# Optimization experiments

Hardware: AMD Instinct MI355X
Metric: run time of the kernel (lower is better)

The kernel has to match this reference:

```python
import math
import jax, jax.numpy as jnp
import numpy as np

NHEAD = 4
EPS = 1e-5


def make_pe(max_len, d):
    pos = np.arange(max_len, dtype=np.float32)[:, None]
    div = np.exp(np.arange(0, d, 2, dtype=np.float32) * (-math.log(10000.0) / d))
    pe = np.zeros((max_len, d), np.float32)
    pe[:, 0::2] = np.sin(pos * div)
    pe[:, 1::2] = np.cos(pos * div)
    return jnp.asarray(pe)


def layer_norm(x, g, b):
    m = jnp.mean(x, axis=-1, keepdims=True)
    v = jnp.mean((x - m) ** 2, axis=-1, keepdims=True)
    return (x - m) / jnp.sqrt(v + EPS) * g + b


def mha(q, k, v, wq, bq, wk, bk, wv, bv, wo, bo, kmask=None):
    # q: [b, Lq, d], k/v: [b, Lk, d]
    b_, lq, d = q.shape
    lk = k.shape[1]
    hd = d // NHEAD
    qh = (q @ wq + bq).reshape(b_, lq, NHEAD, hd)
    kh = (k @ wk + bk).reshape(b_, lk, NHEAD, hd)
    vh = (v @ wv + bv).reshape(b_, lk, NHEAD, hd)
    s = jnp.einsum('bqhd,bkhd->bhqk', qh, kh) / jnp.sqrt(jnp.float32(hd))
    if kmask is not None:
        s = jnp.where(kmask[None, None, None, :], s, jnp.float32(-1e9))
    a = jax.nn.softmax(s, axis=-1)
    o = jnp.einsum('bhqk,bkhd->bqhd', a, vh).reshape(b_, lq, d)
    return o @ wo + bo


def _forward(src, in_w, in_b, dec_start,
             e_wq, e_bq, e_wk, e_bk, e_wv, e_bv, e_wo, e_bo,
             e_ln1_g, e_ln1_b, e_w1, e_b1, e_w2, e_b2, e_ln2_g, e_ln2_b,
             d_swq, d_sbq, d_swk, d_sbk, d_swv, d_sbv, d_swo, d_sbo,
             d_ln1_g, d_ln1_b,
             d_cwq, d_cbq, d_cwk, d_cbk, d_cwv, d_cbv, d_cwo, d_cbo,
             d_ln2_g, d_ln2_b,
             d_w1, d_b1, d_w2, d_b2, d_ln3_g, d_ln3_b,
             out_w, out_b, tgt_len):
    B, S = src.shape
    d = in_w.shape[1]
    T = tgt_len
    pe = make_pe(max(S, T) + 10, d)

    # ---- encoder (1 post-norm layer, relu FFN, dropout off) ----
    x = (src[..., None] @ in_w + in_b) * jnp.sqrt(jnp.float32(d))  # [B,S,d]
    x = x + pe[None, :S]
    x = layer_norm(x + mha(x, x, x, e_wq, e_bq, e_wk, e_bk, e_wv, e_bv, e_wo, e_bo), e_ln1_g, e_ln1_b)
    mem = layer_norm(x + (jax.nn.relu(x @ e_w1 + e_b1) @ e_w2 + e_b2), e_ln2_g, e_ln2_b)

    buf0 = jnp.zeros((B, T + 1, d), src.dtype).at[:, 0].set(dec_start[0, 0])
    pe_dec = pe[None, :T + 1]
    kidx = jnp.arange(T + 1)

    def step(buf, t):
        di = buf + pe_dec
        kmask = kidx <= t  # full (non-causal) attention over the t+1 valid tokens
        h = layer_norm(di + mha(di, di, di, d_swq, d_sbq, d_swk, d_sbk,
                                d_swv, d_sbv, d_swo, d_sbo, kmask=kmask),
                       d_ln1_g, d_ln1_b)
        h = layer_norm(h + mha(h, mem, mem, d_cwq, d_cbq, d_cwk, d_cbk,
                               d_cwv, d_cbv, d_cwo, d_cbo),
                       d_ln2_g, d_ln2_b)
        h = layer_norm(h + (jax.nn.relu(h @ d_w1 + d_b1) @ d_w2 + d_b2),
                       d_ln3_g, d_ln3_b)
        last = h[:, t]                       # [B,d] output at the newest position
        buf = buf.at[:, t + 1].set(last)     # feed back as next decoder token
        y = (last @ out_w + out_b)[:, 0]     # [B]
        return buf, y

    _, outs = jax.lax.scan(step, buf0, jnp.arange(T))  # outs: [T,B]
    return outs.T  # [B,T]


def setup_inputs():
    B, S, T, d, ff = 128, 512, 64, 48, 128
    ks = iter(jax.random.split(jax.random.key(0), 64))

    def w(shape, s=0.08):
        return jax.random.normal(next(ks), shape, jnp.float32) * s

    ones = lambda: jnp.ones((d,), jnp.float32)
    zeros = lambda: jnp.zeros((d,), jnp.float32)
    return dict(
        src=jax.random.normal(next(ks), (B, S), jnp.float32),
        in_w=w((1, d)), in_b=w((d,)),
        dec_start=w((1, 1, d), 1.0),
        e_wq=w((d, d)), e_bq=w((d,)), e_wk=w((d, d)), e_bk=w((d,)),
        e_wv=w((d, d)), e_bv=w((d,)), e_wo=w((d, d)), e_bo=w((d,)),
        e_ln1_g=ones(), e_ln1_b=zeros(),
        e_w1=w((d, ff)), e_b1=w((ff,)), e_w2=w((ff, d)), e_b2=w((d,)),
        e_ln2_g=ones(), e_ln2_b=zeros(),
        d_swq=w((d, d)), d_sbq=w((d,)), d_swk=w((d, d)), d_sbk=w((d,)),
        d_swv=w((d, d)), d_sbv=w((d,)), d_swo=w((d, d)), d_sbo=w((d,)),
        d_ln1_g=ones(), d_ln1_b=zeros(),
        d_cwq=w((d, d)), d_cbq=w((d,)), d_cwk=w((d, d)), d_cbk=w((d,)),
        d_cwv=w((d, d)), d_cbv=w((d,)), d_cwo=w((d, d)), d_cbo=w((d,)),
        d_ln2_g=ones(), d_ln2_b=zeros(),
        d_w1=w((d, ff)), d_b1=w((ff,)), d_w2=w((ff, d)), d_b2=w((d,)),
        d_ln3_g=ones(), d_ln3_b=zeros(),
        out_w=w((d, 1)), out_b=w((1,)),
        tgt_len=T,
    )


def reference(src, in_w, in_b, dec_start,
              e_wq, e_bq, e_wk, e_bk, e_wv, e_bv, e_wo, e_bo,
              e_ln1_g, e_ln1_b, e_w1, e_b1, e_w2, e_b2, e_ln2_g, e_ln2_b,
              d_swq, d_sbq, d_swk, d_sbk, d_swv, d_sbv, d_swo, d_sbo,
              d_ln1_g, d_ln1_b,
              d_cwq, d_cbq, d_cwk, d_cbk, d_cwv, d_cbv, d_cwo, d_cbo,
              d_ln2_g, d_ln2_b,
              d_w1, d_b1, d_w2, d_b2, d_ln3_g, d_ln3_b,
              out_w, out_b, tgt_len):
    return _forward(src, in_w, in_b, dec_start,
                    e_wq, e_bq, e_wk, e_bk, e_wv, e_bv, e_wo, e_bo,
                    e_ln1_g, e_ln1_b, e_w1, e_b1, e_w2, e_b2, e_ln2_g, e_ln2_b,
                    d_swq, d_sbq, d_swk, d_sbk, d_swv, d_sbv, d_swo, d_sbo,
                    d_ln1_g, d_ln1_b,
                    d_cwq, d_cbq, d_cwk, d_cbk, d_cwv, d_cbv, d_cwo, d_cbo,
                    d_ln2_g, d_ln2_b,
                    d_w1, d_b1, d_w2, d_b2, d_ln3_g, d_ln3_b,
                    out_w, out_b, tgt_len)
```

## Files before the change

### kernel.cpp

```cpp
#include <hip/hip_runtime.h>
#include <hip/hip_bf16.h>
#include <hip/hip_fp16.h>


constexpr int kB  = 128;
constexpr int kS  = 512;
constexpr int kT  = 64;
constexpr int kD  = 48;
constexpr int kFF = 128;
constexpr int kNH = 4;
constexpr int kHD = 12;

__device__ __forceinline__ void wsync(){
  __builtin_amdgcn_wave_barrier();
  asm volatile("" ::: "memory");
}

template<int CTRL,int RM,int BM,bool BC>
__device__ __forceinline__ float dppmov(float x, float old){
  return __builtin_bit_cast(float, __builtin_amdgcn_update_dpp(
      __builtin_bit_cast(int, old), __builtin_bit_cast(int, x), CTRL, RM, BM, BC));
}
__device__ __forceinline__ float wsum(float x){
  x += dppmov<0x111,0xf,0xf,true>(x, 0.f);
  x += dppmov<0x112,0xf,0xf,true>(x, 0.f);
  x += dppmov<0x114,0xf,0xf,true>(x, 0.f);
  x += dppmov<0x118,0xf,0xf,true>(x, 0.f);
  x += dppmov<0x142,0xa,0xf,true>(x, 0.f);
  x += dppmov<0x143,0xc,0xf,true>(x, 0.f);
  return __builtin_bit_cast(float, __builtin_amdgcn_readlane(__builtin_bit_cast(int, x), 63));
}
__device__ __forceinline__ float rowsum16(float x){
  x += dppmov<0x111,0xf,0xf,true>(x, 0.f);
  x += dppmov<0x112,0xf,0xf,true>(x, 0.f);
  x += dppmov<0x114,0xf,0xf,true>(x, 0.f);
  x += dppmov<0x118,0xf,0xf,true>(x, 0.f);
  return x;
}

__device__ __forceinline__ float pe_val(int p, int j){
  int i = j >> 1;
  float f = expf(-0.19188209108283716f * (float)(2*i));
  float a = (float)p * f;
  return (j & 1) ? cosf(a) : sinf(a);
}
__device__ __forceinline__ float pe_fast(int p, int j){
  int i = j >> 1;
  float f = __expf(-0.19188209108283716f * (float)(2*i));
  float a = (float)p * f;
  return (j & 1) ? __cosf(a) : __sinf(a);
}

typedef _Float16 h2v __attribute__((ext_vector_type(2)));
union H2U { __half2 h; h2v v; };
__device__ __forceinline__ float fdot2(__half2 a, __half2 b, float c){
#if __has_builtin(__builtin_amdgcn_fdot2)
  H2U ua, ub; ua.h=a; ub.h=b;
  return __builtin_amdgcn_fdot2(ua.v, ub.v, c, false);
#else
  float2 fa=__half22float2(a), fb=__half22float2(b);
  return fmaf(fa.y, fb.y, fmaf(fa.x, fb.x, c));
#endif
}
union F4H2 { float4 f; __half2 h[4]; };

__device__ __forceinline__ float dot48d(const __half2* x, const __half* w){
  const __half2* w2=(const __half2*)w;
  float a0=0.f,a1=0.f,a2=0.f,a3=0.f;
  #pragma unroll
  for(int c=0;c<6;c++){
    a0=fdot2(x[4*c+0],w2[4*c+0],a0);
    a1=fdot2(x[4*c+1],w2[4*c+1],a1);
    a2=fdot2(x[4*c+2],w2[4*c+2],a2);
    a3=fdot2(x[4*c+3],w2[4*c+3],a3);
  }
  return (a0+a1)+(a2+a3);
}
__device__ __forceinline__ float dot128d(const __half2* x, const __half* w){
  const __half2* w2=(const __half2*)w;
  float a0=0.f,a1=0.f,a2=0.f,a3=0.f,a4=0.f,a5=0.f,a6=0.f,a7=0.f;
  #pragma unroll
  for(int c=0;c<8;c++){
    a0=fdot2(x[8*c+0],w2[8*c+0],a0);
    a1=fdot2(x[8*c+1],w2[8*c+1],a1);
    a2=fdot2(x[8*c+2],w2[8*c+2],a2);
    a3=fdot2(x[8*c+3],w2[8*c+3],a3);
    a4=fdot2(x[8*c+4],w2[8*c+4],a4);
    a5=fdot2(x[8*c+5],w2[8*c+5],a5);
    a6=fdot2(x[8*c+6],w2[8*c+6],a6);
    a7=fdot2(x[8*c+7],w2[8*c+7],a7);
  }
  return ((a0+a1)+(a2+a3))+((a4+a5)+(a6+a7));
}

__global__ void __launch_bounds__(256) k_qkv(const float* __restrict__ src,
    const float* __restrict__ in_w, const float* __restrict__ in_b,
    float* __restrict__ X0,
    const float* __restrict__ wq, const float* __restrict__ bq,
    const float* __restrict__ wk, const float* __restrict__ bk,
    const float* __restrict__ wv, const float* __restrict__ bv,
    __half* __restrict__ Q, __half* __restrict__ K, __half* __restrict__ V,
    const float* __restrict__ swq, const float* __restrict__ swk,
    const float* __restrict__ swv, const float* __restrict__ swo,
    const float* __restrict__ cwq, const float* __restrict__ cwo,
    const float* __restrict__ dw1, const float* __restrict__ dw2,
    __half* __restrict__ Wh){
  if(blockIdx.x >= 2048){
    int idx=(blockIdx.x-2048)*256+threadIdx.x;
    if(idx>=26112) return;
    if(idx<13824){
      int m=idx/2304, e=idx%2304, j=e/48, k=e%48;
      const float* w = (m==0)?swq:((m==1)?swk:((m==2)?swv:((m==3)?swo:((m==4)?cwq:cwo))));
      Wh[m*2688 + j*56 + k] = __float2half(w[k*48+j]);
    } else if(idx<19968){
      int e=idx-13824, c=e/48, k=e%48;
      Wh[16128 + c*56 + k] = __float2half(dw1[k*128+c]);
    } else {
      int e=idx-19968, j=e/128, u=e%128;
      Wh[23296 + j*136 + u] = __float2half(dw2[u*48+j]);
    }
    return;
  }
  __shared__ __align__(16) __half W[3*2688];
  __shared__ __align__(16) float bias[3*kD];
  __shared__ __align__(16) __half2 xt2[32*24];
  int tid = threadIdx.x;
  for (int i=tid;i<3*2304;i+=256){ int m=i/2304, e=i%2304, k=e/48, j=e%48;
    const float* w = (m==0)?wq:((m==1)?wk:wv);
    W[m*2688 + j*56 + k] = __float2half(w[e]); }
  for (int i=tid;i<3*kD;i+=256){ int m=i/kD,e=i%kD;
    const float* w=(m==0)?bq:((m==1)?bk:bv); bias[i]=w[e]; }
  long row0 = (long)blockIdx.x*32;
  const float sc = 6.928203230275509f;
  for (int i=tid;i<768;i+=256){
    int r=i/24, c=i%24;
    long gr=row0+r; int s=(int)(gr&511);
    float sv=src[gr];
    float va=(sv*in_w[2*c  ]+in_b[2*c  ])*sc + pe_fast(s,2*c  );
    float vb=(sv*in_w[2*c+1]+in_b[2*c+1])*sc + pe_fast(s,2*c+1);
    ((float2*)X0)[row0*24 + i]=make_float2(va,vb);
    xt2[i]=__floats2half2_rn(va,vb);
  }
  __syncthreads();
  int r = tid>>3, c0 = tid&7;
  __half2 xr[24];
  #pragma unroll
  for(int u=0;u<24;u++) xr[u]=xt2[r*24+u];
  const float rs = 0.28867513459481287f;
  for (int c=c0; c<3*kD; c+=8){
    int m=c/kD, j=c%kD;
    float acc = bias[m*kD+j] + dot48d(xr, W + m*2688 + j*56);
    if(m==0) acc*=rs;
    __half* o = (m==0)?Q:((m==1)?K:V);
    o[(row0+r)*kD+j]=__float2half(acc);
  }
}

__global__ void __launch_bounds__(256) k_attn(const __half* __restrict__ Q,
      const __half* __restrict__ K, const __half* __restrict__ V,
      __half* __restrict__ OP, float* __restrict__ lP){
  int part = blockIdx.x & 1;
  int bh = blockIdx.x >> 1;
  int b = bh / kNH, h = bh % kNH;
  __shared__ __align__(16) __half2 Ks2[256*8];
  __shared__ __align__(16) float   Vs[256*kHD];
  int tid = threadIdx.x;
  long base = ((long)b*kS)*kD + h*kHD;
  int k0 = part<<8;
  for (int i=tid;i<256*6;i+=256){ int r=i/6, c=i%6;
    Ks2[r*8+c]=*(const __half2*)&K[base+(long)(k0+r)*kD+2*c]; }
  for (int i=tid;i<256*kHD;i+=256){ int r=i/kHD, d=i%kHD;
    Vs[i]=__half2float(V[base+(long)(k0+r)*kD+d]); }
  int q0 = tid, q1 = tid+256;
  __half2 qa2[6], qb2[6];
  {
    const __half2* qp0=(const __half2*)(Q+base+(long)q0*kD);
    const __half2* qp1=(const __half2*)(Q+base+(long)q1*kD);
    #pragma unroll
    for(int c=0;c<6;c++){ qa2[c]=qp0[c]; qb2[c]=qp1[c]; }
  }
  __syncthreads();
  float2 acc0[6], acc1[6];
  #pragma unroll
  for(int j=0;j<6;j++){ acc0[j]=make_float2(0.f,0.f); acc1[j]=make_float2(0.f,0.f); }
  float l0=0.f, l1=0.f;
  for(int k=0;k<256;k++){
    const float4* kp4=(const float4*)(Ks2+k*8);
    F4H2 u0,u1; u0.f=kp4[0]; u1.f=kp4[1];
    float sA0=0.f,sA1=0.f,sB0=0.f,sB1=0.f;
    sA0=fdot2(qa2[0],u0.h[0],sA0); sA1=fdot2(qa2[1],u0.h[1],sA1);
    sA0=fdot2(qa2[2],u0.h[2],sA0); sA1=fdot2(qa2[3],u0.h[3],sA1);
    sA0=fdot2(qa2[4],u1.h[0],sA0); sA1=fdot2(qa2[5],u1.h[1],sA1);
    sB0=fdot2(qb2[0],u0.h[0],sB0); sB1=fdot2(qb2[1],u0.h[1],sB1);
    sB0=fdot2(qb2[2],u0.h[2],sB0); sB1=fdot2(qb2[3],u0.h[3],sB1);
    sB0=fdot2(qb2[4],u1.h[0],sB0); sB1=fdot2(qb2[5],u1.h[1],sB1);
    float p0=__expf(sA0+sA1), p1=__expf(sB0+sB1);
    l0+=p0; l1+=p1;
    const float4* vp=(const float4*)(Vs+k*kHD);
    float4 v0=vp[0], v1=vp[1], v2=vp[2];
    acc0[0].x=fmaf(p0,v0.x,acc0[0].x); acc0[0].y=fmaf(p0,v0.y,acc0[0].y);
    acc0[1].x=fmaf(p0,v0.z,acc0[1].x); acc0[1].y=fmaf(p0,v0.w,acc0[1].y);
    acc0[2].x=fmaf(p0,v1.x,acc0[2].x); acc0[2].y=fmaf(p0,v1.y,acc0[2].y);
    acc0[3].x=fmaf(p0,v1.z,acc0[3].x); acc0[3].y=fmaf(p0,v1.w,acc0[3].y);
    acc0[4].x=fmaf(p0,v2.x,acc0[4].x); acc0[4].y=fmaf(p0,v2.y,acc0[4].y);
    acc0[5].x=fmaf(p0,v2.z,acc0[5].x); acc0[5].y=fmaf(p0,v2.w,acc0[5].y);
    acc1[0].x=fmaf(p1,v0.x,acc1[0].x); acc1[0].y=fmaf(p1,v0.y,acc1[0].y);
    acc1[1].x=fmaf(p1,v0.z,acc1[1].x); acc1[1].y=fmaf(p1,v0.w,acc1[1].y);
    acc1[2].x=fmaf(p1,v1.x,acc1[2].x); acc1[2].y=fmaf(p1,v1.y,acc1[2].y);
    acc1[3].x=fmaf(p1,v1.z,acc1[3].x); acc1[3].y=fmaf(p1,v1.w,acc1[3].y);
    acc1[4].x=fmaf(p1,v2.x,acc1[4].x); acc1[4].y=fmaf(p1,v2.y,acc1[4].y);
    acc1[5].x=fmaf(p1,v2.z,acc1[5].x); acc1[5].y=fmaf(p1,v2.w,acc1[5].y);
  }
  float i0=1.f/l0, i1=1.f/l1;
  const long PS=(long)kB*kNH*kS*kHD, LS=(long)kB*kNH*kS;
  long ob=((long)(b*kNH+h))*kS;
  __half2* op0=(__half2*)(OP + part*PS + (ob+q0)*kHD);
  __half2* op1=(__half2*)(OP + part*PS + (ob+q1)*kHD);
  #pragma unroll
  for(int j=0;j<6;j++){
    op0[j]=__floats2half2_rn(acc0[j].x*i0, acc0[j].y*i0);
    op1[j]=__floats2half2_rn(acc1[j].x*i1, acc1[j].y*i1);
  }
  lP[part*LS + ob + q0]=l0;
  lP[part*LS + ob + q1]=l1;
}

__global__ void __launch_bounds__(256) k_oproj_ln(const float* __restrict__ Xres,
      const __half* __restrict__ OP, const float* __restrict__ lP,
      const float* __restrict__ wo, const float* __restrict__ bo,
      const float* __restrict__ g, const float* __restrict__ bb,
      __half* __restrict__ Xout){
  __shared__ __align__(16) __half W[kD*56];
  __shared__ float bsh[kD], gs[kD], bs2[kD];
  __shared__ __align__(16) float res[32*kD];
  __shared__ __align__(16) __half2 ot2[32*24];
  __shared__ float mrow[32], rstd[32];
  int tid=threadIdx.x;
  for(int i=tid;i<kD*kD;i+=256){ int k=i/48, j=i%48; W[j*56+k]=__float2half(wo[i]); }
  if(tid<kD){ bsh[tid]=bo[tid]; gs[tid]=g[tid]; bs2[tid]=bb[tid]; }
  long row0=(long)blockIdx.x*32;
  const long PS=(long)kB*kNH*kS*kHD, LS=(long)kB*kNH*kS;
  for(int i=tid;i<768;i+=256){
    int r=i/24, c=i%24;
    long gq=row0+r; long bb2=gq>>9; long s=gq&511;
    int h=c/6; int d0=(2*c)%12;
    long li=(bb2*kNH+h)*kS+s;
    float l0=lP[li], l1=lP[li+LS];
    float inv=1.f/(l0+l1);
    long o0=li*(long)kHD+d0;
    float v0=(l0*__half2float(OP[o0  ]) + l1*__half2float(OP[o0  +PS]))*inv;
    float v1=(l0*__half2float(OP[o0+1]) + l1*__half2float(OP[o0+1+PS]))*inv;
    ot2[i]=__floats2half2_rn(v0,v1);
  }
  __syncthreads();
  int r=tid>>3, c0=tid&7;
  __half2 orow[24];
  #pragma unroll
  for(int u=0;u<24;u++) orow[u]=ot2[r*24+u];
  for(int j=c0;j<kD;j+=8){
    float acc=bsh[j]+dot48d(orow, W+j*56);
    res[r*kD+j]=Xres[row0*kD + r*kD + j]+acc;
  }
  __syncthreads();
  if(tid<32){
    float s=0.f, s2=0.f;
    for(int j=0;j<kD;j++){ float v=res[tid*kD+j]; s+=v; s2+=v*v; }
    float m=s*(1.f/kD);
    mrow[tid]=m; rstd[tid]=rsqrtf(s2*(1.f/kD)-m*m+1e-5f);
  }
  __syncthreads();
  for(int i=tid;i<32*kD;i+=256){int r2=i/kD,j=i%kD;
    Xout[row0*kD+i]=__float2half((res[i]-mrow[r2])*rstd[r2]*gs[j]+bs2[j]); }
}

__global__ void __launch_bounds__(256) k_ffn_ln(const __half* __restrict__ Xin,
   const float* __restrict__ w1, const float* __restrict__ b1,
   const float* __restrict__ w2, const float* __restrict__ b2,
   const float* __restrict__ g, const float* __restrict__ bb,
   float* __restrict__ Xout){
  __shared__ __align__(16) __half W1[kFF*56];
  __shared__ __align__(16) __half W2[kD*136];
  __shared__ float b1s[kFF], b2s[kD], gs[kD], bs2[kD];
  __shared__ __align__(16) __half xt[16*kD];
  __shared__ __align__(16) __half h1h[16*kFF];
  __shared__ __align__(16) float res[16*kD];
  __shared__ float mrow[16], rstd[16];
  int tid=threadIdx.x;
  for(int i=tid;i<kD*kFF;i+=256){ int k=i/128, c=i%128; W1[c*56+k]=__float2half(w1[i]); }
  for(int i=tid;i<kFF*kD;i+=256){ int u=i/48, j=i%48; W2[j*136+u]=__float2half(w2[i]); }
  if(tid<kFF) b1s[tid]=b1[tid];
  if(tid<kD){ b2s[tid]=b2[tid]; gs[tid]=g[tid]; bs2[tid]=bb[tid]; }
  long row0=(long)blockIdx.x*16;
  const __half2* Xp=(const __half2*)(Xin+row0*kD);
  for(int i=tid;i<384;i+=256) ((__half2*)xt)[i]=Xp[i];
  __syncthreads();
  int r=tid>>4, c0=tid&15;
  {
    __half2 xr[24];
    const __half2* xp=(const __half2*)(xt + r*kD);
    #pragma unroll
    for(int u=0;u<24;u++) xr[u]=xp[u];
    for(int c=c0;c<kFF;c+=16){
      float acc=b1s[c]+dot48d(xr, W1+c*56);
      h1h[r*kFF+c]=__float2half(fmaxf(acc,0.f));
    }
  }
  __syncthreads();
  {
    const __half2* hp=(const __half2*)(h1h + r*kFF);
    for(int j=c0;j<kD;j+=16){
      float acc=b2s[j]+dot128d(hp, W2+j*136);
      res[r*kD+j]=__half2float(xt[r*kD+j])+acc;
    }
  }
  __syncthreads();
  if(tid<16){
    float s=0.f, s2=0.f;
    for(int j=0;j<kD;j++){ float v=res[tid*kD+j]; s+=v; s2+=v*v; }
    float m=s*(1.f/kD);
    mrow[tid]=m; rstd[tid]=rsqrtf(s2*(1.f/kD)-m*m+1e-5f);
  }
  __syncthreads();
  for(int i=tid;i<16*kD;i+=256){int r2=i/kD,j=i%kD;
    Xout[row0*kD+i]=(res[i]-mrow[r2])*rstd[r2]*gs[j]+bs2[j]; }
}

__global__ void __launch_bounds__(256) k_ckv(const float* __restrict__ M,
    const float* __restrict__ wk, const float* __restrict__ bk,
    const float* __restrict__ wv, const float* __restrict__ bv,
    __half* __restrict__ Kc, __half* __restrict__ Vc){
  __shared__ __align__(16) __half W[2*2688];
  __shared__ float bias[2*kD];
  __shared__ __align__(16) __half2 xt2[32*24];
  int tid=threadIdx.x;
  for(int i=tid;i<2*2304;i+=256){ int m=i/2304, e=i%2304, k=e/48, j=e%48;
    W[m*2688 + j*56 + k] = __float2half((m?wv:wk)[e]); }
  for(int i=tid;i<2*kD;i+=256){ int m=i/kD,e=i%kD; bias[i]=(m?bv:bk)[e]; }
  long row0=(long)blockIdx.x*32;
  const float2* Mp=(const float2*)(M+row0*kD);
  for(int i=tid;i<768;i+=256){ float2 v=Mp[i]; xt2[i]=__floats2half2_rn(v.x,v.y); }
  __syncthreads();
  int r=tid>>3, c0=tid&7;
  __half2 xr[24];
  #pragma unroll
  for(int u=0;u<24;u++) xr[u]=xt2[r*24+u];
  long gr=row0+r; long bb2=gr>>9; long s=gr&511;
  for(int c=c0;c<2*kD;c+=8){
    int m=c/kD, j=c%kD;
    float acc=bias[m*kD+j]+dot48d(xr, W+m*2688+j*56);
    if(m==0) Kc[(bb2*kS+s)*kD + j]=__float2half(acc);
    else     Vc[(bb2*kD+j)*kS + s]=__float2half(acc);
  }
}

struct DecP {
  const float *dec_start, *sbq, *sbk, *sbv, *sbo, *ln1g, *ln1b,
              *cbq, *cbo, *ln2g, *ln2b, *fb1, *fb2, *ln3g, *ln3b, *ow, *ob;
};

__global__ void __launch_bounds__(256,1) k_dec(const __half* __restrict__ KT,
    const __half* __restrict__ VT, const __half* __restrict__ Wg, DecP P,
    float* __restrict__ out){
  __shared__ __align__(16) __half Wl[29824];
  __shared__ __align__(16) float peT[kT*kD];
  __shared__ __align__(16) __half KhH[kNH*kT*kHD];
  __shared__ __align__(16) float  Vh[kNH*kT*kHD];
  __shared__ __align__(16) __half qSH[kNH*kHD];
  __shared__ __align__(16) float poS[kNH][kD];
  __shared__ __align__(16) __half xvH[kD], soH[kD], h1H[kD], cqH[kD], h2H[kD];
  __shared__ __align__(16) __half f1H[kFF];
  int tid=threadIdx.x, b=blockIdx.x, wave=tid>>6, lane=tid&63;
  const float rs=0.28867513459481287f;

  for(int i=tid;i<29824/8;i+=256) ((float4*)Wl)[i]=((const float4*)Wg)[i];
  for(int i=tid;i<kT*kD;i+=256){ int tt=i/kD, j=i%kD; peT[i]=pe_val(tt,j); }

  float c_sbq=0,c_sbk=0,c_sbv=0, c_bo=0,c_cbq=0,c_cbo=0,c_fb2=0;
  float g1=0,bb1=0,g2=0,bb2=0,g3=0,bb3=0,c_ow=0, c_fb1a=0,c_fb1b=0, c_ds=0;
  if(wave==0){
    if(lane<kD){
      c_ds=P.dec_start[lane];
      c_sbq=P.sbq[lane]; c_sbk=P.sbk[lane]; c_sbv=P.sbv[lane];
      c_bo=P.sbo[lane]; c_cbq=P.cbq[lane]; c_cbo=P.cbo[lane]; c_fb2=P.fb2[lane];
      g1=P.ln1g[lane]; bb1=P.ln1b[lane];
      g2=P.ln2g[lane]; bb2=P.ln2b[lane];
      g3=P.ln3g[lane]; bb3=P.ln3b[lane];
      c_ow=P.ow[lane];
    }
    c_fb1a=P.fb1[lane]; c_fb1b=P.fb1[lane+64];
  }
  float c_ob=P.ob[0];

  __half2 Kr2[4][2][6], Vr2[4][kHD];
  {
    const __half* Kb = KT + (long)b*kS*kD;
    const __half2* Vb = (const __half2*)VT + (long)b*kD*(kS/2);
    #pragma unroll
    for(int i=0;i<4;i++){
      int sp = lane + 64*i;
      #pragma unroll
      for(int e=0;e<2;e++){
        const __half2* kp=(const __half2*)(Kb + (long)(2*sp+e)*kD + wave*kHD);
        #pragma unroll
        for(int c=0;c<6;c++) Kr2[i][e][c]=kp[c];
      }
      #pragma unroll
// ... 126 lines not shown
    __syncthreads();
    if(wave==0){
      {
        float rr=0.f;
        if(lane<kD)
          rr=h1+c_cbo+((poS[0][lane]+poS[1][lane])+(poS[2][lane]+poS[3][lane]));
        float s1=wsum(rr), s2=wsum(rr*rr);
        float mean=s1*(1.f/48.f);
        float rstd=rsqrtf(s2*(1.f/48.f)-mean*mean+1e-5f);
        h2=0;
        if(lane<kD){ h2=(rr-mean)*rstd*g2+bb2; h2H[lane]=__float2half(h2); }
      }
      wsync();
      {
        float a=c_fb1a+dot48d((const __half2*)h2H, Wl+16128+lane*56);
        float bcol=c_fb1b+dot48d((const __half2*)h2H, Wl+16128+(lane+64)*56);
        f1H[lane]=__float2half(fmaxf(a,0.f));
        f1H[lane+64]=__float2half(fmaxf(bcol,0.f));
      }
      wsync();
      {
        float rr=0.f;
        if(lane<kD)
          rr=h2+c_fb2+dot128d((const __half2*)f1H, Wl+23296+lane*136);
        float s1=wsum(rr), s2=wsum(rr*rr);
        float mean=s1*(1.f/48.f);
        float rstd=rsqrtf(s2*(1.f/48.f)-mean*mean+1e-5f);
        float cv=0.f;
        if(lane<kD) cv=(rr-mean)*rstd*g3+bb3;
        if(lane<kD && t+1<kT){ xv=cv+peT[(t+1)*kD+lane]; xvH[lane]=__float2half(xv); }
        wsync();
        float y=wsum(cv*c_ow);
        if(lane==t) yacc=y;
      }
    }
  }
  if(wave==0) out[(long)b*kT+lane]=yacc+c_ob;
}

extern "C" void kernel_launch(void* const* d_in, const int* in_sizes, int n_in,
                              void* d_out, int out_size, void* d_ws, size_t ws_size,
                              hipStream_t stream){
  float* ws = (float*)d_ws;
  __half* Wh = (__half*)ws;
  const size_t NB = (size_t)kB*kS*kD;
  const size_t BHS = (size_t)kB*kNH*kS;
  float*  A  = ws + 16384;
  __half* H1 = (__half*)(A + NB);
  __half* H2 = H1 + NB;
  __half* H3 = H2 + NB;
  __half* OP = H3 + NB;
  float*  lP = (float*)(OP + 2*NB);

  k_qkv  <<<2048+102,256,0,stream>>>((const float*)d_in[0],(const float*)d_in[1],(const float*)d_in[2],A,
                                     (const float*)d_in[4],(const float*)d_in[5],(const float*)d_in[6],
                                     (const float*)d_in[7],(const float*)d_in[8],(const float*)d_in[9],H1,H2,H3,
                                     (const float*)d_in[20],(const float*)d_in[22],(const float*)d_in[24],
                                     (const float*)d_in[26],(const float*)d_in[30],(const float*)d_in[36],
                                     (const float*)d_in[40],(const float*)d_in[42],Wh);
  k_attn <<<kB*kNH*2,256,0,stream>>>(H1,H2,H3,OP,lP);
  k_oproj_ln<<<(kB*kS)/32,256,0,stream>>>(A,OP,lP,(const float*)d_in[10],(const float*)d_in[11],
                                          (const float*)d_in[12],(const float*)d_in[13],H2);
  k_ffn_ln  <<<(kB*kS)/16,256,0,stream>>>(H2,(const float*)d_in[14],(const float*)d_in[15],(const float*)d_in[16],
                                          (const float*)d_in[17],(const float*)d_in[18],(const float*)d_in[19],A);
  k_ckv     <<<(kB*kS)/32,256,0,stream>>>(A,(const float*)d_in[32],(const float*)d_in[33],
                                          (const float*)d_in[34],(const float*)d_in[35],H1,H3);
  DecP P;
  P.dec_start=(const float*)d_in[3];
  P.sbq=(const float*)d_in[21]; P.sbk=(const float*)d_in[23]; P.sbv=(const float*)d_in[25]; P.sbo=(const float*)d_in[27];
  P.ln1g=(const float*)d_in[28]; P.ln1b=(const float*)d_in[29];
  P.cbq=(const float*)d_in[31]; P.cbo=(const float*)d_in[37];
  P.ln2g=(const float*)d_in[38]; P.ln2b=(const float*)d_in[39];
  P.fb1=(const float*)d_in[41]; P.fb2=(const float*)d_in[43];
  P.ln3g=(const float*)d_in[44]; P.ln3b=(const float*)d_in[45];
  P.ow=(const float*)d_in[46]; P.ob=(const float*)d_in[47];
  k_dec<<<kB,256,0,stream>>>(H1,H3,Wh,P,(float*)d_out);
}
```

Baseline: 567.3 us.

## Fuse encoder kernels into one persistent cooperative kernel with grid syncs

The five encoder kernels (QKV projection, attention, output projection + LayerNorm, FFN + LayerNorm, cross-attention K/V projection) become phases of one persistent cooperative kernel. It launches 768 blocks that loop over tiles and separate the phases with grid-wide syncs. This removes inter-kernel launch gaps and stages each phase's fp16 weights into shared memory once per block instead of once per tile. The trade-off is a 38 KB shared arena that caps occupancy, grid-sync cost, and uneven work in the attention phase (1024 items over 768 blocks). If the cooperative launch fails, it falls back to separate kernel launches.

```diff
diff --git a/kernel.cpp b/kernel.cpp
--- a/kernel.cpp
+++ b/kernel.cpp
@@ -1,6 +1,9 @@
 #include <hip/hip_runtime.h>
+#include <hip/hip_cooperative_groups.h>
 #include <hip/hip_bf16.h>
 #include <hip/hip_fp16.h>
+
+namespace cg = cooperative_groups;
 
 
 constexpr int kB  = 128;
@@ -93,265 +96,296 @@
   return ((a0+a1)+(a2+a3))+((a4+a5)+(a6+a7));
 }
 
-__global__ void __launch_bounds__(256) k_qkv(const float* __restrict__ src,
-    const float* __restrict__ in_w, const float* __restrict__ in_b,
-    float* __restrict__ X0,
-    const float* __restrict__ wq, const float* __restrict__ bq,
-    const float* __restrict__ wk, const float* __restrict__ bk,
-    const float* __restrict__ wv, const float* __restrict__ bv,
-    __half* __restrict__ Q, __half* __restrict__ K, __half* __restrict__ V,
-    const float* __restrict__ swq, const float* __restrict__ swk,
-    const float* __restrict__ swv, const float* __restrict__ swo,
-    const float* __restrict__ cwq, const float* __restrict__ cwo,
-    const float* __restrict__ dw1, const float* __restrict__ dw2,
-    __half* __restrict__ Wh){
-  if(blockIdx.x >= 2048){
-    int idx=(blockIdx.x-2048)*256+threadIdx.x;
-    if(idx>=26112) return;
+constexpr int kArena = 38400;
+
+struct EncP {
+  const float *src,*in_w,*in_b; float* X0;
+  const float *wq,*bq,*wk,*bk,*wv,*bv;
+  __half *Q,*K,*V;
+  const float *swq,*swk,*swv,*swo,*cwq,*cwo,*dw1,*dw2; __half* Wh;
+  __half* OP; float* lP;
+  const float *wo,*bo,*g1,*b1g; __half* X1;
+  const float *w1,*b1,*w2,*b2,*g2,*b2g; float* Xm;
+  const float *ckw,*ckb,*cvw,*cvb; __half *Kc,*Vc;
+};
+
+__device__ __forceinline__ void phase_qkv(unsigned char* arena, const EncP& p){
+  __half* W=(__half*)arena;
+  float* bias=(float*)(arena+16128);
+  __half2* xt2=(__half2*)(arena+16704);
+  int tid=threadIdx.x;
+  for(int i=tid;i<3*2304;i+=256){ int m=i/2304,e=i%2304,k=e/48,j=e%48;
+    const float* w=(m==0)?p.wq:((m==1)?p.wk:p.wv);
+    W[m*2688+j*56+k]=__float2half(w[e]); }
+  for(int i=tid;i<3*kD;i+=256){ int m=i/kD,e=i%kD;
+    const float* w=(m==0)?p.bq:((m==1)?p.bk:p.bv); bias[i]=w[e]; }
+  for(int idx=blockIdx.x*256+tid; idx<26112; idx+=gridDim.x*256){
     if(idx<13824){
-      int m=idx/2304, e=idx%2304, j=e/48, k=e%48;
-      const float* w = (m==0)?swq:((m==1)?swk:((m==2)?swv:((m==3)?swo:((m==4)?cwq:cwo))));
-      Wh[m*2688 + j*56 + k] = __float2half(w[k*48+j]);
+      int m=idx/2304,e=idx%2304,j=e/48,k=e%48;
+      const float* w=(m==0)?p.swq:((m==1)?p.swk:((m==2)?p.swv:((m==3)?p.swo:((m==4)?p.cwq:p.cwo))));
+      p.Wh[m*2688+j*56+k]=__float2half(w[k*48+j]);
     } else if(idx<19968){
-      int e=idx-13824, c=e/48, k=e%48;
-      Wh[16128 + c*56 + k] = __float2half(dw1[k*128+c]);
+      int e=idx-13824,c=e/48,k=e%48;
+      p.Wh[16128+c*56+k]=__float2half(p.dw1[k*128+c]);
     } else {
-      int e=idx-19968, j=e/128, u=e%128;
-      Wh[23296 + j*136 + u] = __float2half(dw2[u*48+j]);
-    }
-    return;
-  }
-  __shared__ __align__(16) __half W[3*2688];
-  __shared__ __align__(16) float bias[3*kD];
-  __shared__ __align__(16) __half2 xt2[32*24];
-  int tid = threadIdx.x;
-  for (int i=tid;i<3*2304;i+=256){ int m=i/2304, e=i%2304, k=e/48, j=e%48;
-    const float* w = (m==0)?wq:((m==1)?wk:wv);
-    W[m*2688 + j*56 + k] = __float2half(w[e]); }
-  for (int i=tid;i<3*kD;i+=256){ int m=i/kD,e=i%kD;
-    const float* w=(m==0)?bq:((m==1)?bk:bv); bias[i]=w[e]; }
-  long row0 = (long)blockIdx.x*32;
-  const float sc = 6.928203230275509f;
-  for (int i=tid;i<768;i+=256){
-    int r=i/24, c=i%24;
-    long gr=row0+r; int s=(int)(gr&511);
-    float sv=src[gr];
-    float va=(sv*in_w[2*c  ]+in_b[2*c  ])*sc + pe_fast(s,2*c  );
-    float vb=(sv*in_w[2*c+1]+in_b[2*c+1])*sc + pe_fast(s,2*c+1);
-    ((float2*)X0)[row0*24 + i]=make_float2(va,vb);
-    xt2[i]=__floats2half2_rn(va,vb);
-  }
-  __syncthreads();
-  int r = tid>>3, c0 = tid&7;
-  __half2 xr[24];
-  #pragma unroll
-  for(int u=0;u<24;u++) xr[u]=xt2[r*24+u];
-  const float rs = 0.28867513459481287f;
-  for (int c=c0; c<3*kD; c+=8){
-    int m=c/kD, j=c%kD;
-    float acc = bias[m*kD+j] + dot48d(xr, W + m*2688 + j*56);
-    if(m==0) acc*=rs;
-    __half* o = (m==0)?Q:((m==1)?K:V);
-    o[(row0+r)*kD+j]=__float2half(acc);
-  }
-}
-
-__global__ void __launch_bounds__(256) k_attn(const __half* __restrict__ Q,
-      const __half* __restrict__ K, const __half* __restrict__ V,
-      __half* __restrict__ OP, float* __restrict__ lP){
-  int part = blockIdx.x & 1;
-  int bh = blockIdx.x >> 1;
-  int b = bh / kNH, h = bh % kNH;
-  __shared__ __align__(16) __half2 Ks2[256*8];
-  __shared__ __align__(16) float   Vs[256*kHD];
-  int tid = threadIdx.x;
-  long base = ((long)b*kS)*kD + h*kHD;
-  int k0 = part<<8;
-  for (int i=tid;i<256*6;i+=256){ int r=i/6, c=i%6;
-    Ks2[r*8+c]=*(const __half2*)&K[base+(long)(k0+r)*kD+2*c]; }
-  for (int i=tid;i<256*kHD;i+=256){ int r=i/kHD, d=i%kHD;
-    Vs[i]=__half2float(V[base+(long)(k0+r)*kD+d]); }
-  int q0 = tid, q1 = tid+256;
-  __half2 qa2[6], qb2[6];
-  {
-    const __half2* qp0=(const __half2*)(Q+base+(long)q0*kD);
-    const __half2* qp1=(const __half2*)(Q+base+(long)q1*kD);
+      int e=idx-19968,j=e/128,u=e%128;
+      p.Wh[23296+j*136+u]=__float2half(p.dw2[u*48+j]);
+    }
+  }
+  const float sc=6.928203230275509f, rs=0.28867513459481287f;
+  for(long tile=blockIdx.x; tile<2048; tile+=gridDim.x){
+    __syncthreads();
+    long row0=tile*32;
+    for(int i=tid;i<768;i+=256){
+      int r=i/24,c=i%24;
+      long gr=row0+r; int s=(int)(gr&511);
+      float sv=p.src[gr];
+      float va=(sv*p.in_w[2*c  ]+p.in_b[2*c  ])*sc+pe_fast(s,2*c  );
+      float vb=(sv*p.in_w[2*c+1]+p.in_b[2*c+1])*sc+pe_fast(s,2*c+1);
+      ((float2*)p.X0)[row0*24+i]=make_float2(va,vb);
+      xt2[i]=__floats2half2_rn(va,vb);
+    }
+    __syncthreads();
+    int r=tid>>3,c0=tid&7;
+    __half2 xr[24];
     #pragma unroll
-    for(int c=0;c<6;c++){ qa2[c]=qp0[c]; qb2[c]=qp1[c]; }
-  }
-  __syncthreads();
-  float2 acc0[6], acc1[6];
-  #pragma unroll
-  for(int j=0;j<6;j++){ acc0[j]=make_float2(0.f,0.f); acc1[j]=make_float2(0.f,0.f); }
-  float l0=0.f, l1=0.f;
-  for(int k=0;k<256;k++){
-    const float4* kp4=(const float4*)(Ks2+k*8);
-    F4H2 u0,u1; u0.f=kp4[0]; u1.f=kp4[1];
-    float sA0=0.f,sA1=0.f,sB0=0.f,sB1=0.f;
-    sA0=fdot2(qa2[0],u0.h[0],sA0); sA1=fdot2(qa2[1],u0.h[1],sA1);
-    sA0=fdot2(qa2[2],u0.h[2],sA0); sA1=fdot2(qa2[3],u0.h[3],sA1);
-    sA0=fdot2(qa2[4],u1.h[0],sA0); sA1=fdot2(qa2[5],u1.h[1],sA1);
-    sB0=fdot2(qb2[0],u0.h[0],sB0); sB1=fdot2(qb2[1],u0.h[1],sB1);
-    sB0=fdot2(qb2[2],u0.h[2],sB0); sB1=fdot2(qb2[3],u0.h[3],sB1);
-    sB0=fdot2(qb2[4],u1.h[0],sB0); sB1=fdot2(qb2[5],u1.h[1],sB1);
-    float p0=__expf(sA0+sA1), p1=__expf(sB0+sB1);
-    l0+=p0; l1+=p1;
-    const float4* vp=(const float4*)(Vs+k*kHD);
-    float4 v0=vp[0], v1=vp[1], v2=vp[2];
-    acc0[0].x=fmaf(p0,v0.x,acc0[0].x); acc0[0].y=fmaf(p0,v0.y,acc0[0].y);
-    acc0[1].x=fmaf(p0,v0.z,acc0[1].x); acc0[1].y=fmaf(p0,v0.w,acc0[1].y);
-    acc0[2].x=fmaf(p0,v1.x,acc0[2].x); acc0[2].y=fmaf(p0,v1.y,acc0[2].y);
-    acc0[3].x=fmaf(p0,v1.z,acc0[3].x); acc0[3].y=fmaf(p0,v1.w,acc0[3].y);
-    acc0[4].x=fmaf(p0,v2.x,acc0[4].x); acc0[4].y=fmaf(p0,v2.y,acc0[4].y);
-    acc0[5].x=fmaf(p0,v2.z,acc0[5].x); acc0[5].y=fmaf(p0,v2.w,acc0[5].y);
-    acc1[0].x=fmaf(p1,v0.x,acc1[0].x); acc1[0].y=fmaf(p1,v0.y,acc1[0].y);
-    acc1[1].x=fmaf(p1,v0.z,acc1[1].x); acc1[1].y=fmaf(p1,v0.w,acc1[1].y);
-    acc1[2].x=fmaf(p1,v1.x,acc1[2].x); acc1[2].y=fmaf(p1,v1.y,acc1[2].y);
-    acc1[3].x=fmaf(p1,v1.z,acc1[3].x); acc1[3].y=fmaf(p1,v1.w,acc1[3].y);
-    acc1[4].x=fmaf(p1,v2.x,acc1[4].x); acc1[4].y=fmaf(p1,v2.y,acc1[4].y);
-    acc1[5].x=fmaf(p1,v2.z,acc1[5].x); acc1[5].y=fmaf(p1,v2.w,acc1[5].y);
-  }
-  float i0=1.f/l0, i1=1.f/l1;
+    for(int u=0;u<24;u++) xr[u]=xt2[r*24+u];
+    for(int c=c0;c<3*kD;c+=8){
+      int m=c/kD,j=c%kD;
+      float acc=bias[m*kD+j]+dot48d(xr,W+m*2688+j*56);
+      if(m==0) acc*=rs;
+      __half* o=(m==0)?p.Q:((m==1)?p.K:p.V);
+      o[(row0+r)*kD+j]=__float2half(acc);
+    }
+  }
+}
+
+__device__ __forceinline__ void phase_attn(unsigned char* arena, const EncP& p){
+  __half2* Ks2=(__half2*)arena;
+  float*   Vs =(float*)(arena+8192);
+  int tid=threadIdx.x;
   const long PS=(long)kB*kNH*kS*kHD, LS=(long)kB*kNH*kS;
-  long ob=((long)(b*kNH+h))*kS;
-  __half2* op0=(__half2*)(OP + part*PS + (ob+q0)*kHD);
-  __half2* op1=(__half2*)(OP + part*PS + (ob+q1)*kHD);
-  #pragma unroll
-  for(int j=0;j<6;j++){
-    op0[j]=__floats2half2_rn(acc0[j].x*i0, acc0[j].y*i0);
-    op1[j]=__floats2half2_rn(acc1[j].x*i1, acc1[j].y*i1);
-  }
-  lP[part*LS + ob + q0]=l0;
-  lP[part*LS + ob + q1]=l1;
-}
-
-__global__ void __launch_bounds__(256) k_oproj_ln(const float* __restrict__ Xres,
-      const __half* __restrict__ OP, const float* __restrict__ lP,
-      const float* __restrict__ wo, const float* __restrict__ bo,
-      const float* __restrict__ g, const float* __restrict__ bb,
-      __half* __restrict__ Xout){
-  __shared__ __align__(16) __half W[kD*56];
-  __shared__ float bsh[kD], gs[kD], bs2[kD];
-  __shared__ __align__(16) float res[32*kD];
-  __shared__ __align__(16) __half2 ot2[32*24];
-  __shared__ float mrow[32], rstd[32];
+  for(int item=blockIdx.x; item<kB*kNH*2; item+=gridDim.x){
+    __syncthreads();
+    int part=item&1; int bh=item>>1;
+    int b=bh/kNH, h=bh%kNH;
+    long base=((long)b*kS)*kD + h*kHD;
+    int k0=part<<8;
+    for(int i=tid;i<256*6;i+=256){ int r=i/6,c=i%6;
+      Ks2[r*8+c]=*(const __half2*)&p.K[base+(long)(k0+r)*kD+2*c]; }
+    for(int i=tid;i<256*kHD;i+=256){ int r=i/kHD,d=i%kHD;
+      Vs[i]=__half2float(p.V[base+(long)(k0+r)*kD+d]); }
+    int q0=tid, q1=tid+256;
+    __half2 qa2[6], qb2[6];
+    {
+      const __half2* qp0=(const __half2*)(p.Q+base+(long)q0*kD);
+      const __half2* qp1=(const __half2*)(p.Q+base+(long)q1*kD);
+      #pragma unroll
+      for(int c=0;c<6;c++){ qa2[c]=qp0[c]; qb2[c]=qp1[c]; }
+    }
+    __syncthreads();
+    float2 acc0[6], acc1[6];
+    #pragma unroll
+    for(int j=0;j<6;j++){ acc0[j]=make_float2(0.f,0.f); acc1[j]=make_float2(0.f,0.f); }
+    float l0=0.f, l1=0.f;
+    for(int k=0;k<256;k++){
+      const float4* kp4=(const float4*)(Ks2+k*8);
+      F4H2 u0,u1; u0.f=kp4[0]; u1.f=kp4[1];
+      float sA0=0.f,sA1=0.f,sB0=0.f,sB1=0.f;
+      sA0=fdot2(qa2[0],u0.h[0],sA0); sA1=fdot2(qa2[1],u0.h[1],sA1);
+      sA0=fdot2(qa2[2],u0.h[2],sA0); sA1=fdot2(qa2[3],u0.h[3],sA1);
+      sA0=fdot2(qa2[4],u1.h[0],sA0); sA1=fdot2(qa2[5],u1.h[1],sA1);
+      sB0=fdot2(qb2[0],u0.h[0],sB0); sB1=fdot2(qb2[1],u0.h[1],sB1);
+      sB0=fdot2(qb2[2],u0.h[2],sB0); sB1=fdot2(qb2[3],u0.h[3],sB1);
+      sB0=fdot2(qb2[4],u1.h[0],sB0); sB1=fdot2(qb2[5],u1.h[1],sB1);
+      float p0=__expf(sA0+sA1), p1=__expf(sB0+sB1);
+      l0+=p0; l1+=p1;
+      const float4* vp=(const float4*)(Vs+k*kHD);
+      float4 v0=vp[0], v1=vp[1], v2=vp[2];
+      acc0[0].x=fmaf(p0,v0.x,acc0[0].x); acc0[0].y=fmaf(p0,v0.y,acc0[0].y);
+      acc0[1].x=fmaf(p0,v0.z,acc0[1].x); acc0[1].y=fmaf(p0,v0.w,acc0[1].y);
+      acc0[2].x=fmaf(p0,v1.x,acc0[2].x); acc0[2].y=fmaf(p0,v1.y,acc0[2].y);
+      acc0[3].x=fmaf(p0,v1.z,acc0[3].x); acc0[3].y=fmaf(p0,v1.w,acc0[3].y);
+      acc0[4].x=fmaf(p0,v2.x,acc0[4].x); acc0[4].y=fmaf(p0,v2.y,acc0[4].y);
+      acc0[5].x=fmaf(p0,v2.z,acc0[5].x); acc0[5].y=fmaf(p0,v2.w,acc0[5].y);
+      acc1[0].x=fmaf(p1,v0.x,acc1[0].x); acc1[0].y=fmaf(p1,v0.y,acc1[0].y);
+      acc1[1].x=fmaf(p1,v0.z,acc1[1].x); acc1[1].y=fmaf(p1,v0.w,acc1[1].y);
+      acc1[2].x=fmaf(p1,v1.x,acc1[2].x); acc1[2].y=fmaf(p1,v1.y,acc1[2].y);
+      acc1[3].x=fmaf(p1,v1.z,acc1[3].x); acc1[3].y=fmaf(p1,v1.w,acc1[3].y);
+      acc1[4].x=fmaf(p1,v2.x,acc1[4].x); acc1[4].y=fmaf(p1,v2.y,acc1[4].y);
+      acc1[5].x=fmaf(p1,v2.z,acc1[5].x); acc1[5].y=fmaf(p1,v2.w,acc1[5].y);
+    }
+    float i0=1.f/l0, i1=1.f/l1;
+    long ob=((long)(b*kNH+h))*kS;
+    __half2* op0=(__half2*)(p.OP + part*PS + (ob+q0)*kHD);
+    __half2* op1=(__half2*)(p.OP + part*PS + (ob+q1)*kHD);
+    #pragma unroll
+    for(int j=0;j<6;j++){
+      op0[j]=__floats2half2_rn(acc0[j].x*i0, acc0[j].y*i0);
+      op1[j]=__floats2half2_rn(acc1[j].x*i1, acc1[j].y*i1);
+    }
+    p.lP[part*LS + ob + q0]=l0;
+    p.lP[part*LS + ob + q1]=l1;
+  }
+}
+
+__device__ __forceinline__ void phase_oproj(unsigned char* arena, const EncP& p){
+  __half* W=(__half*)arena;
+  float* bsh=(float*)(arena+5376);
+  float* gs =(float*)(arena+5568);
+  float* bs2=(float*)(arena+5760);
+  __half2* ot2=(__half2*)(arena+5952);
+  float* res=(float*)(arena+9024);
+  float* mrow=(float*)(arena+15168);
+  float* rstd=(float*)(arena+15296);
   int tid=threadIdx.x;
-  for(int i=tid;i<kD*kD;i+=256){ int k=i/48, j=i%48; W[j*56+k]=__float2half(wo[i]); }
-  if(tid<kD){ bsh[tid]=bo[tid]; gs[tid]=g[tid]; bs2[tid]=bb[tid]; }
-  long row0=(long)blockIdx.x*32;
+  for(int i=tid;i<kD*kD;i+=256){int k=i/48,j=i%48; W[j*56+k]=__float2half(p.wo[i]);}
+  if(tid<kD){ bsh[tid]=p.bo[tid]; gs[tid]=p.g1[tid]; bs2[tid]=p.b1g[tid]; }
   const long PS=(long)kB*kNH*kS*kHD, LS=(long)kB*kNH*kS;
-  for(int i=tid;i<768;i+=256){
-    int r=i/24, c=i%24;
-    long gq=row0+r; long bb2=gq>>9; long s=gq&511;
-    int h=c/6; int d0=(2*c)%12;
-    long li=(bb2*kNH+h)*kS+s;
-    float l0=lP[li], l1=lP[li+LS];
-    float inv=1.f/(l0+l1);
-    long o0=li*(long)kHD+d0;
-    float v0=(l0*__half2float(OP[o0  ]) + l1*__half2float(OP[o0  +PS]))*inv;
-    float v1=(l0*__half2float(OP[o0+1]) + l1*__half2float(OP[o0+1+PS]))*inv;
-    ot2[i]=__floats2half2_rn(v0,v1);
-  }
-  __syncthreads();
-  int r=tid>>3, c0=tid&7;
-  __half2 orow[24];
-  #pragma unroll
-  for(int u=0;u<24;u++) orow[u]=ot2[r*24+u];
-  for(int j=c0;j<kD;j+=8){
-    float acc=bsh[j]+dot48d(orow, W+j*56);
-    res[r*kD+j]=Xres[row0*kD + r*kD + j]+acc;
-  }
-  __syncthreads();
-  if(tid<32){
-    float s=0.f, s2=0.f;
-    for(int j=0;j<kD;j++){ float v=res[tid*kD+j]; s+=v; s2+=v*v; }
-    float m=s*(1.f/kD);
-    mrow[tid]=m; rstd[tid]=rsqrtf(s2*(1.f/kD)-m*m+1e-5f);
-  }
-  __syncthreads();
-  for(int i=tid;i<32*kD;i+=256){int r2=i/kD,j=i%kD;
-    Xout[row0*kD+i]=__float2half((res[i]-mrow[r2])*rstd[r2]*gs[j]+bs2[j]); }
-}
-
-__global__ void __launch_bounds__(256) k_ffn_ln(const __half* __restrict__ Xin,
-   const float* __restrict__ w1, const float* __restrict__ b1,
-   const float* __restrict__ w2, const float* __restrict__ b2,
-   const float* __restrict__ g, const float* __restrict__ bb,
-   float* __restrict__ Xout){
-  __shared__ __align__(16) __half W1[kFF*56];
-  __shared__ __align__(16) __half W2[kD*136];
-  __shared__ float b1s[kFF], b2s[kD], gs[kD], bs2[kD];
-  __shared__ __align__(16) __half xt[16*kD];
-  __shared__ __align__(16) __half h1h[16*kFF];
-  __shared__ __align__(16) float res[16*kD];
-  __shared__ float mrow[16], rstd[16];
+  for(long tile=blockIdx.x; tile<2048; tile+=gridDim.x){
+    __syncthreads();
+    long row0=tile*32;
+    for(int i=tid;i<768;i+=256){
+      int r=i/24,c=i%24;
+      long gq=row0+r; long bb2=gq>>9; long s=gq&511;
+      int h=c/6; int d0=(2*c)%12;
+      long li=(bb2*kNH+h)*kS+s;
+      float l0=p.lP[li], l1=p.lP[li+LS];
+      float inv=1.f/(l0+l1);
+      long o0=li*(long)kHD+d0;
+      float v0=(l0*__half2float(p.OP[o0  ])+l1*__half2float(p.OP[o0  +PS]))*inv;
+      float v1=(l0*__half2float(p.OP[o0+1])+l1*__half2float(p.OP[o0+1+PS]))*inv;
+      ot2[i]=__floats2half2_rn(v0,v1);
+    }
+    __syncthreads();
+    int r=tid>>3,c0=tid&7;
+    __half2 orow[24];
+    #pragma unroll
+    for(int u=0;u<24;u++) orow[u]=ot2[r*24+u];
+    for(int j=c0;j<kD;j+=8){
+      float acc=bsh[j]+dot48d(orow,W+j*56);
+      res[r*kD+j]=p.X0[row0*kD+r*kD+j]+acc;
+    }
+    __syncthreads();
+    if(tid<32){
+      float s=0.f,s2=0.f;
+      for(int j=0;j<kD;j++){float v=res[tid*kD+j]; s+=v; s2+=v*v;}
+      float m=s*(1.f/kD);
+      mrow[tid]=m; rstd[tid]=rsqrtf(s2*(1.f/kD)-m*m+1e-5f);
+    }
+    __syncthreads();
+    for(int i=tid;i<32*kD;i+=256){int r2=i/kD,j=i%kD;
+      p.X1[row0*kD+i]=__float2half((res[i]-mrow[r2])*rstd[r2]*gs[j]+bs2[j]);}
+  }
+}
+
+__device__ __forceinline__ void phase_ffn(unsigned char* arena, const EncP& p){
+  __half* W1=(__half*)arena;
+  __half* W2=(__half*)(arena+14336);
+  float* b1s=(float*)(arena+27392);
+  float* b2s=(float*)(arena+27904);
+  float* gs =(float*)(arena+28096);
+  float* bs2=(float*)(arena+28288);
+  __half* xt=(__half*)(arena+28480);
+  __half* h1h=(__half*)(arena+30016);
+  float* res=(float*)(arena+34112);
+  float* mrow=(float*)(arena+37184);
+  float* rstd=(float*)(arena+37248);
   int tid=threadIdx.x;
-  for(int i=tid;i<kD*kFF;i+=256){ int k=i/128, c=i%128; W1[c*56+k]=__float2half(w1[i]); }
-  for(int i=tid;i<kFF*kD;i+=256){ int u=i/48, j=i%48; W2[j*136+u]=__float2half(w2[i]); }
-  if(tid<kFF) b1s[tid]=b1[tid];
-  if(tid<kD){ b2s[tid]=b2[tid]; gs[tid]=g[tid]; bs2[tid]=bb[tid]; }
-  long row0=(long)blockIdx.x*16;
-  const __half2* Xp=(const __half2*)(Xin+row0*kD);
-  for(int i=tid;i<384;i+=256) ((__half2*)xt)[i]=Xp[i];
-  __syncthreads();
-  int r=tid>>4, c0=tid&15;
-  {
+  for(int i=tid;i<kD*kFF;i+=256){ int k=i/128,c=i%128; W1[c*56+k]=__float2half(p.w1[i]); }
+  for(int i=tid;i<kFF*kD;i+=256){ int u=i/48,j=i%48; W2[j*136+u]=__float2half(p.w2[i]); }
+  if(tid<kFF) b1s[tid]=p.b1[tid];
+  if(tid<kD){ b2s[tid]=p.b2[tid]; gs[tid]=p.g2[tid]; bs2[tid]=p.b2g[tid]; }
+  for(long tile=blockIdx.x; tile<4096; tile+=gridDim.x){
+    __syncthreads();
+    long row0=tile*16;
+    const __half2* Xp=(const __half2*)(p.X1+row0*kD);
+    for(int i=tid;i<384;i+=256) ((__half2*)xt)[i]=Xp[i];
+    __syncthreads();
+    int r=tid>>4,c0=tid&15;
+    {
+      __half2 xr[24];
+      const __half2* xp=(const __half2*)(xt+r*kD);
+      #pragma unroll
+      for(int u=0;u<24;u++) xr[u]=xp[u];
+      for(int c=c0;c<kFF;c+=16){
+        float acc=b1s[c]+dot48d(xr,W1+c*56);
+        h1h[r*kFF+c]=__float2half(fmaxf(acc,0.f));
+      }
+    }
+    __syncthreads();
+    {
+      const __half2* hp=(const __half2*)(h1h+r*kFF);
+      for(int j=c0;j<kD;j+=16){
+        float acc=b2s[j]+dot128d(hp,W2+j*136);
+        res[r*kD+j]=__half2float(xt[r*kD+j])+acc;
+      }
+    }
+    __syncthreads();
+    if(tid<16){
+      float s=0.f,s2=0.f;
+      for(int j=0;j<kD;j++){float v=res[tid*kD+j]; s+=v; s2+=v*v;}
+      float m=s*(1.f/kD);
+      mrow[tid]=m; rstd[tid]=rsqrtf(s2*(1.f/kD)-m*m+1e-5f);
+    }
+    __syncthreads();
+    for(int i=tid;i<16*kD;i+=256){int r2=i/kD,j=i%kD;
+      p.Xm[row0*kD+i]=(res[i]-mrow[r2])*rstd[r2]*gs[j]+bs2[j];}
+  }
+}
+
+__device__ __forceinline__ void phase_ckv(unsigned char* arena, const EncP& p){
+  __half* W=(__half*)arena;
+  float* bias=(float*)(arena+10752);
+  __half2* xt2=(__half2*)(arena+11136);
+  int tid=threadIdx.x;
+  for(int i=tid;i<2*2304;i+=256){ int m=i/2304,e=i%2304,k=e/48,j=e%48;
+    W[m*2688+j*56+k]=__float2half((m?p.cvw:p.ckw)[e]); }
+  for(int i=tid;i<2*kD;i+=256){ int m=i/kD,e=i%kD; bias[i]=(m?p.cvb:p.ckb)[e]; }
+  for(long tile=blockIdx.x; tile<2048; tile+=gridDim.x){
+    __syncthreads();
+    long row0=tile*32;
+    const float2* Mp=(const float2*)(p.Xm+row0*kD);
+    for(int i=tid;i<768;i+=256){ float2 v=Mp[i]; xt2[i]=__floats2half2_rn(v.x,v.y); }
+    __syncthreads();
+    int r=tid>>3,c0=tid&7;
     __half2 xr[24];
-    const __half2* xp=(const __half2*)(xt + r*kD);
     #pragma unroll
-    for(int u=0;u<24;u++) xr[u]=xp[u];
-    for(int c=c0;c<kFF;c+=16){
-      float acc=b1s[c]+dot48d(xr, W1+c*56);
-      h1h[r*kFF+c]=__float2half(fmaxf(acc,0.f));
-    }
-  }
-  __syncthreads();
-  {
-    const __half2* hp=(const __half2*)(h1h + r*kFF);
-    for(int j=c0;j<kD;j+=16){
-      float acc=b2s[j]+dot128d(hp, W2+j*136);
-      res[r*kD+j]=__half2float(xt[r*kD+j])+acc;
-    }
-  }
-  __syncthreads();
-  if(tid<16){
-    float s=0.f, s2=0.f;
-    for(int j=0;j<kD;j++){ float v=res[tid*kD+j]; s+=v; s2+=v*v; }
-    float m=s*(1.f/kD);
-    mrow[tid]=m; rstd[tid]=rsqrtf(s2*(1.f/kD)-m*m+1e-5f);
-  }
-  __syncthreads();
-  for(int i=tid;i<16*kD;i+=256){int r2=i/kD,j=i%kD;
-    Xout[row0*kD+i]=(res[i]-mrow[r2])*rstd[r2]*gs[j]+bs2[j]; }
-}
-
-__global__ void __launch_bounds__(256) k_ckv(const float* __restrict__ M,
-    const float* __restrict__ wk, const float* __restrict__ bk,
-    const float* __restrict__ wv, const float* __restrict__ bv,
-    __half* __restrict__ Kc, __half* __restrict__ Vc){
-  __shared__ __align__(16) __half W[2*2688];
-  __shared__ float bias[2*kD];
-  __shared__ __align__(16) __half2 xt2[32*24];
-  int tid=threadIdx.x;
-  for(int i=tid;i<2*2304;i+=256){ int m=i/2304, e=i%2304, k=e/48, j=e%48;
-    W[m*2688 + j*56 + k] = __float2half((m?wv:wk)[e]); }
-  for(int i=tid;i<2*kD;i+=256){ int m=i/kD,e=i%kD; bias[i]=(m?bv:bk)[e]; }
-  long row0=(long)blockIdx.x*32;
-  const float2* Mp=(const float2*)(M+row0*kD);
-  for(int i=tid;i<768;i+=256){ float2 v=Mp[i]; xt2[i]=__floats2half2_rn(v.x,v.y); }
-  __syncthreads();
-  int r=tid>>3, c0=tid&7;
-  __half2 xr[24];
-  #pragma unroll
-  for(int u=0;u<24;u++) xr[u]=xt2[r*24+u];
-  long gr=row0+r; long bb2=gr>>9; long s=gr&511;
-  for(int c=c0;c<2*kD;c+=8){
-    int m=c/kD, j=c%kD;
-    float acc=bias[m*kD+j]+dot48d(xr, W+m*2688+j*56);
-    if(m==0) Kc[(bb2*kS+s)*kD + j]=__float2half(acc);
-    else     Vc[(bb2*kD+j)*kS + s]=__float2half(acc);
-  }
-}
+    for(int u=0;u<24;u++) xr[u]=xt2[r*24+u];
+    long gr=row0+r; long bb2=gr>>9; long s=gr&511;
+    for(int c=c0;c<2*kD;c+=8){
+      int m=c/kD,j=c%kD;
+      float acc=bias[m*kD+j]+dot48d(xr,W+m*2688+j*56);
+      if(m==0) p.Kc[(bb2*kS+s)*kD+j]=__float2half(acc);
+      else     p.Vc[(bb2*kD+j)*kS+s]=__float2half(acc);
+    }
+  }
+}
+
+__global__ void __launch_bounds__(256,3) k_enc(EncP p){
+  __shared__ __align__(16) unsigned char arena[kArena];
+  cg::grid_group g = cg::this_grid();
+  phase_qkv(arena, p);
+  g.sync();
+  phase_attn(arena, p);
+  g.sync();
+  phase_oproj(arena, p);
+  g.sync();
+  phase_ffn(arena, p);
+  g.sync();
+  phase_ckv(arena, p);
+}
+
+__global__ void __launch_bounds__(256) k_qkv_w(EncP p){
+  __shared__ __align__(16) unsigned char arena[kArena]; phase_qkv(arena,p); }
+__global__ void __launch_bounds__(256) k_attn_w(EncP p){
+  __shared__ __align__(16) unsigned char arena[kArena]; phase_attn(arena,p); }
+__global__ void __launch_bounds__(256) k_oproj_w(EncP p){
+  __shared__ __align__(16) unsigned char arena[kArena]; phase_oproj(arena,p); }
+__global__ void __launch_bounds__(256) k_ffn_w(EncP p){
+  __shared__ __align__(16) unsigned char arena[kArena]; phase_ffn(arena,p); }
+__global__ void __launch_bounds__(256) k_ckv_w(EncP p){
+  __shared__ __align__(16) unsigned char arena[kArena]; phase_ckv(arena,p); }
 
 struct DecP {
   const float *dec_start, *sbq, *sbk, *sbv, *sbo, *ln1g, *ln1b,
@@ -584,19 +618,36 @@
   __half* OP = H3 + NB;
   float*  lP = (float*)(OP + 2*NB);
 
-  k_qkv  <<<2048+102,256,0,stream>>>((const float*)d_in[0],(const float*)d_in[1],(const float*)d_in[2],A,
-                                     (const float*)d_in[4],(const float*)d_in[5],(const float*)d_in[6],
-                                     (const float*)d_in[7],(const float*)d_in[8],(const float*)d_in[9],H1,H2,H3,
-                                     (const float*)d_in[20],(const float*)d_in[22],(const float*)d_in[24],
-                                     (const float*)d_in[26],(const float*)d_in[30],(const float*)d_in[36],
-                                     (const float*)d_in[40],(const float*)d_in[42],Wh);
-  k_attn <<<kB*kNH*2,256,0,stream>>>(H1,H2,H3,OP,lP);
-  k_oproj_ln<<<(kB*kS)/32,256,0,stream>>>(A,OP,lP,(const float*)d_in[10],(const float*)d_in[11],
-                                          (const float*)d_in[12],(const float*)d_in[13],H2);
-  k_ffn_ln  <<<(kB*kS)/16,256,0,stream>>>(H2,(const float*)d_in[14],(const float*)d_in[15],(const float*)d_in[16],
-                                          (const float*)d_in[17],(const float*)d_in[18],(const float*)d_in[19],A);
-  k_ckv     <<<(kB*kS)/32,256,0,stream>>>(A,(const float*)d_in[32],(const float*)d_in[33],
-                                          (const float*)d_in[34],(const float*)d_in[35],H1,H3);
+  EncP e;
+  e.src=(const float*)d_in[0]; e.in_w=(const float*)d_in[1]; e.in_b=(const float*)d_in[2]; e.X0=A;
+  e.wq=(const float*)d_in[4]; e.bq=(const float*)d_in[5];
+  e.wk=(const float*)d_in[6]; e.bk=(const float*)d_in[7];
+  e.wv=(const float*)d_in[8]; e.bv=(const float*)d_in[9];
+  e.Q=H1; e.K=H2; e.V=H3;
+  e.swq=(const float*)d_in[20]; e.swk=(const float*)d_in[22]; e.swv=(const float*)d_in[24];
+  e.swo=(const float*)d_in[26]; e.cwq=(const float*)d_in[30]; e.cwo=(const float*)d_in[36];
+  e.dw1=(const float*)d_in[40]; e.dw2=(const float*)d_in[42]; e.Wh=Wh;
+  e.OP=OP; e.lP=lP;
+  e.wo=(const float*)d_in[10]; e.bo=(const float*)d_in[11];
+  e.g1=(const float*)d_in[12]; e.b1g=(const float*)d_in[13]; e.X1=H2;
+  e.w1=(const float*)d_in[14]; e.b1=(const float*)d_in[15];
+  e.w2=(const float*)d_in[16]; e.b2=(const float*)d_in[17];
+  e.g2=(const float*)d_in[18]; e.b2g=(const float*)d_in[19]; e.Xm=A;
+  e.ckw=(const float*)d_in[32]; e.ckb=(const float*)d_in[33];
+  e.cvw=(const float*)d_in[34]; e.cvb=(const float*)d_in[35];
+  e.Kc=H1; e.Vc=H3;
+
+  void* args[] = { (void*)&e };
+  hipError_t err = hipLaunchCooperativeKernel((void*)k_enc, dim3(768), dim3(256),
+                                              args, 0, stream);
+  if(err != hipSuccess){
+    k_qkv_w  <<<2048,256,0,stream>>>(e);
+    k_attn_w <<<1024,256,0,stream>>>(e);
+    k_oproj_w<<<2048,256,0,stream>>>(e);
+    k_ffn_w  <<<4096,256,0,stream>>>(e);
+    k_ckv_w  <<<2048,256,0,stream>>>(e);
+  }
+
   DecP P;
   P.dec_start=(const float*)d_in[3];
   P.sbq=(const float*)d_in[21]; P.sbk=(const float*)d_in[23]; P.sbv=(const float*)d_in[25]; P.sbo=(const float*)d_in[27];
```

Result: slower. 966.4 us (+70.3%).
